# Optimization experiments

Hardware: AMD Instinct MI355X
Metric: run time of the kernel (lower is better)

## Reference

```python
import jax, jax.numpy as jnp
import numpy as np

EMB_DIM = 256
NUM_EMB = 2048
COM_COEF = 0.25


def setup_inputs() -> dict:
    key = jax.random.key(0)
    k1, k2 = jax.random.split(key)
    x = jax.random.normal(k1, (64, 32, 32, EMB_DIM), dtype=jnp.float32)
    # VarianceScaling(uniform) over (emb_dim, num_emb): limit = sqrt(3*scale/fan_in)
    limit = float(np.sqrt(3.0 / EMB_DIM))
    codebook = jax.random.uniform(k2, (EMB_DIM, NUM_EMB), dtype=jnp.float32,
                                  minval=-limit, maxval=limit)
    return {"x": x, "codebook": codebook}


def reference(x, codebook):
    original_shape = x.shape
    flat = jnp.reshape(x, (-1, EMB_DIM))  # [N, D]
    sim = jnp.matmul(flat, codebook)
    dists = (jnp.sum(jnp.square(flat), axis=-1, keepdims=True)
             + jnp.sum(jnp.square(codebook), axis=0)
             - 2.0 * sim)
    indexes = jnp.argmin(dists, axis=-1)  # [N]
    encodings = jax.nn.one_hot(indexes, NUM_EMB, dtype=flat.dtype)  # [N, num_emb]
    quantized = jnp.matmul(encodings, codebook.T)  # [N, D]
    quantized = jnp.reshape(quantized, original_shape)

    latent_loss = jnp.square(jax.lax.stop_gradient(x) - quantized)
    commitment_loss = jnp.square(jax.lax.stop_gradient(quantized) - x)
    loss = jnp.mean(latent_loss + COM_COEF * commitment_loss)

    # straight-through estimator
    quantized_st = x + jax.lax.stop_gradient(quantized - x)

    avg_probs = jnp.mean(encodings, axis=0)
    perplexity = jnp.exp(-jnp.sum(avg_probs * jnp.log(avg_probs + 1e-10)))
    return quantized_st, loss, perplexity
```

## Files before the change

kernel.cpp:

```cpp
#include <hip/hip_runtime.h>
#include <hip/hip_fp16.h>
#include <math.h>

#define EMB_DIM 256
#define NUM_EMB 2048
#define N_ROWS  65536
#define N_ELEM  16777216
#define EPS_GAP 8e-3f

#define IDX_OFF    0
#define XSQ_OFF    65536
#define ESQ_OFF    131072
#define ESQH_OFF   133120
#define HIST_OFF   135168
#define BKT_OFF    137216
#define CNT_OFF    137472
#define FLG_OFF    137473
#define CBT_OFF    262144
#define CBTH_OFF   786432

typedef __attribute__((ext_vector_type(8))) _Float16 half8;
typedef __attribute__((ext_vector_type(4))) float f32x4;
typedef unsigned int u32;

__device__ __forceinline__ void gl_lds16(const void* g, void* l) {
    __builtin_amdgcn_global_load_lds(
        (const __attribute__((address_space(1))) u32*)g,
        (__attribute__((address_space(3))) u32*)l, 16, 0, 0);
}

__global__ __launch_bounds__(256) void prep_all(
    const float* __restrict__ x, const float* __restrict__ cb,
    float* __restrict__ esq, float* __restrict__ esqh,
    float* __restrict__ cbT, __half* __restrict__ cbTh,
    __half* __restrict__ xh, float* __restrict__ xsq) {
    __shared__ float lt[64][65];
    const int bid = blockIdx.x;
    const int t = threadIdx.x;
    if (bid < 8) {
        int e = bid * 256 + t;
        float s0 = 0.f, s1 = 0.f, s2 = 0.f, s3 = 0.f;
        float h0 = 0.f, h1 = 0.f, h2 = 0.f, h3 = 0.f;
        for (int d = 0; d < EMB_DIM; d += 4) {
            float c0 = cb[(d + 0) * NUM_EMB + e];
            float c1 = cb[(d + 1) * NUM_EMB + e];
            float c2 = cb[(d + 2) * NUM_EMB + e];
            float c3 = cb[(d + 3) * NUM_EMB + e];
            s0 = fmaf(c0, c0, s0); s1 = fmaf(c1, c1, s1);
            s2 = fmaf(c2, c2, s2); s3 = fmaf(c3, c3, s3);
            float q0 = __half2float(__float2half(c0));
            float q1 = __half2float(__float2half(c1));
            float q2 = __half2float(__float2half(c2));
            float q3 = __half2float(__float2half(c3));
            h0 = fmaf(q0, q0, h0); h1 = fmaf(q1, q1, h1);
            h2 = fmaf(q2, q2, h2); h3 = fmaf(q3, q3, h3);
        }
        esq[e]  = (s0 + s1) + (s2 + s3);
        esqh[e] = (h0 + h1) + (h2 + h3);
    } else if (bid < 136) {
        int b = bid - 8;
        int et = (b & 31) * 64;
        int dt = (b >> 5) * 64;
        #pragma unroll
        for (int p = 0; p < 4; ++p) {
            int d  = p * 16 + (t >> 4);
            int e4 = (t & 15) * 4;
            const float4 v = *(const float4*)&cb[(dt + d) * NUM_EMB + et + e4];
            lt[d][e4] = v.x; lt[d][e4 + 1] = v.y; lt[d][e4 + 2] = v.z; lt[d][e4 + 3] = v.w;
        }
        __syncthreads();
        #pragma unroll
        for (int p = 0; p < 4; ++p) {
            int e  = p * 16 + (t >> 4);
            int d4 = (t & 15) * 4;
            float a[4] = {lt[d4][e], lt[d4 + 1][e], lt[d4 + 2][e], lt[d4 + 3][e]};
            *(float4*)&cbT[(et + e) * EMB_DIM + dt + d4] = make_float4(a[0], a[1], a[2], a[3]);
            unsigned short hb[4];
            #pragma unroll
            for (int i = 0; i < 4; ++i)
                hb[i] = __half_as_ushort(__float2half(a[i]));
            *(ushort4*)&cbTh[(et + e) * EMB_DIM + dt + d4] = make_ushort4(hb[0], hb[1], hb[2], hb[3]);
        }
    } else {
        int b = bid - 136;
        int row = b * 4 + (t >> 6);
        int c = (t & 63) * 4;
        const float4 v = *(const float4*)&x[row * EMB_DIM + c];
        float a[4] = {v.x, v.y, v.z, v.w};
        unsigned short hb[4];
        float s = 0.f;
        #pragma unroll
        for (int i = 0; i < 4; ++i) {
            hb[i] = __half_as_ushort(__float2half(a[i]));
            s = fmaf(a[i], a[i], s);
        }
        *(ushort4*)&xh[row * EMB_DIM + c] = make_ushort4(hb[0], hb[1], hb[2], hb[3]);
        #pragma unroll
        for (int o = 32; o > 0; o >>= 1) s += __shfl_down(s, o, 64);
        if ((t & 63) == 0) xsq[row] = s;
    }
}

#define BUFH 20480
__global__ __launch_bounds__(256, 2) void argmin_mfma(
    const __half* __restrict__ xh_, const __half* __restrict__ cbh_,
    const float* __restrict__ esqh,
    int* __restrict__ idx_out, int* __restrict__ cnt, int* __restrict__ flg) {

    __shared__ _Float16 ldsbuf[2 * BUFH];
    _Float16* lds = ldsbuf;

    const _Float16* xh  = (const _Float16*)xh_;
    const _Float16* cbh = (const _Float16*)cbh_;

    const int t = threadIdx.x;
    const int w = t >> 6, L = t & 63;
    const int wn = w * 64;
    const int lm = L & 15, lq = L >> 4;
    const int ph = (lm >> 1) & 3;
    const int rowbase = blockIdx.x * 64;

    const int srow = L >> 2;
    const int sq   = (L & 3) ^ ((L >> 3) & 3);

    const _Float16* pa  = xh + (size_t)(rowbase + w * 16 + srow) * EMB_DIM + sq * 8;
    const _Float16* pb0 = cbh + (size_t)(w * 16 + srow) * EMB_DIM + sq * 8;
    const int oA = (w * 16) * 32;
    const int oB = (w * 16) * 32;

    float best[16], b2[16];
    int   bi[16];
    #pragma unroll
    for (int s = 0; s < 16; ++s) { best[s] = 3.4e38f; b2[s] = 3.4e38f; bi[s] = 0; }

    #define STAGE(S_, bb) do {                                                   \
        const int nnt_ = (S_) >> 2;                                              \
        const int km_  = ((S_) & 3) * 64;                                        \
        const _Float16* pb_ = pb0 + (size_t)nnt_ * 256 * EMB_DIM + km_;          \
        gl_lds16(pa + km_,                 (bb) + oA);                           \
        gl_lds16(pa + km_ + 32,            (bb) + 2048 + oA);                    \
        gl_lds16(pb_ +   0 * EMB_DIM,      (bb) + 4096 + oB);                    \
        gl_lds16(pb_ +  64 * EMB_DIM,      (bb) + 4096 + oB + 2048);             \
        gl_lds16(pb_ + 128 * EMB_DIM,      (bb) + 4096 + oB + 4096);             \
        gl_lds16(pb_ + 192 * EMB_DIM,      (bb) + 4096 + oB + 6144);             \
        gl_lds16(pb_ +   0 * EMB_DIM + 32, (bb) + 12288 + oB);                   \
        gl_lds16(pb_ +  64 * EMB_DIM + 32, (bb) + 12288 + oB + 2048);            \
        gl_lds16(pb_ + 128 * EMB_DIM + 32, (bb) + 12288 + oB + 4096);            \
        gl_lds16(pb_ + 192 * EMB_DIM + 32, (bb) + 12288 + oB + 6144);            \
    } while (0)

    STAGE(0, lds);

    for (int nt = 0; nt < 8; ++nt) {
        float eq[4];
        #pragma unroll
        for (int g = 0; g < 4; ++g)
            eq[g] = esqh[nt * 256 + wn + g * 16 + lm];

        f32x4 acc[4][4];
        #pragma unroll
        for (int f = 0; f < 4; ++f)
            #pragma unroll
            for (int g = 0; g < 4; ++g)
                acc[f][g] = (f32x4){0.f, 0.f, 0.f, 0.f};

        for (int mt = 0; mt < 4; ++mt) {
            const int S = nt * 4 + mt;

            __builtin_amdgcn_sched_barrier(0);
            asm volatile("s_waitcnt vmcnt(0)" ::: "memory");
            __builtin_amdgcn_s_barrier();
            __builtin_amdgcn_sched_barrier(0);

            if (S < 31)
                STAGE(S + 1, lds + ((S + 1) & 1) * BUFH);

            const _Float16* bb = lds + (S & 1) * BUFH;

            half8 ah[2][4], bh[2][4];
            #pragma unroll
            for (int h = 0; h < 2; ++h)
                #pragma unroll
                for (int f = 0; f < 4; ++f)
                    ah[h][f] = *(const half8*)&bb[h * 2048 + (f * 16 + lm) * 32 + ((lq ^ ph) * 8)];
            #pragma unroll
            for (int h = 0; h < 2; ++h)
                #pragma unroll
                for (int g = 0; g < 4; ++g)
                    bh[h][g] = *(const half8*)&bb[4096 + h * 8192 + (wn + g * 16 + lm) * 32 + ((lq ^ ph) * 8)];

            asm volatile("s_waitcnt lgkmcnt(0)" ::: "memory");
            __builtin_amdgcn_sched_barrier(0);
            __builtin_amdgcn_s_barrier();
            __builtin_amdgcn_sched_barrier(0);

            __builtin_amdgcn_s_setprio(1);
            #pragma unroll
            for (int h = 0; h < 2; ++h)
                #pragma unroll
                for (int f = 0; f < 4; ++f)
                    #pragma unroll
                    for (int g = 0; g < 4; ++g)
                        acc[f][g] = __builtin_amdgcn_mfma_f32_16x16x32_f16(ah[h][f], bh[h][g], acc[f][g], 0, 0, 0);
            __builtin_amdgcn_s_setprio(0);
        }

        #pragma unroll
        for (int g = 0; g < 4; ++g) {
            int col = nt * 256 + wn + g * 16 + lm;
            #pragma unroll
            for (int f = 0; f < 4; ++f)
                #pragma unroll
                for (int r = 0; r < 4; ++r) {
                    int s = f * 4 + r;
                    float v = fmaf(-2.0f, acc[f][g][r], eq[g]);
                    float bo = best[s];
                    b2[s]   = fminf(b2[s], fmaxf(bo, v));
                    best[s] = fminf(bo, v);
                    bi[s]   = (v < bo) ? col : bi[s];
                }
        }
    }
    #undef STAGE

    __syncthreads();
    float* smemf = (float*)ldsbuf;
    float* rd = smemf;
    int*   ri = (int*)(smemf + 4160);
    float* r2 = smemf + 8320;
    #pragma unroll
    for (int f = 0; f < 4; ++f)
        #pragma unroll
        for (int r = 0; r < 4; ++r) {
            int row = f * 16 + lq * 4 + r;
            int c = w * 16 + lm;
            rd[row * 65 + c] = best[f * 4 + r];
            ri[row * 65 + c] = bi[f * 4 + r];
            r2[row * 65 + c] = b2[f * 4 + r];
        }
    __syncthreads();
    if (t < 64) {
        int row = t;
        float g1 = rd[row * 65]; int gi = ri[row * 65]; float g2 = r2[row * 65];
        for (int c = 1; c < 64; ++c) {
            float d = rd[row * 65 + c]; int ic = ri[row * 65 + c]; float d2 = r2[row * 65 + c];
            if (d < g1 || (d == g1 && ic < gi)) { g2 = fminf(g1, d2); g1 = d; gi = ic; }
            else g2 = fminf(g2, d);
        }
        idx_out[rowbase + row] = gi;
        if (g2 - g1 < EPS_GAP) {
            int p = atomicAdd(cnt, 1);
            flg[p] = rowbase + row;
        }
    }
}

__global__ __launch_bounds__(256) void fallback_k(const float* __restrict__ x,
                                                  const float* __restrict__ cb,
                                                  const float* __restrict__ xsq,
                                                  const float* __restrict__ esq,
                                                  const int* __restrict__ cnt,
                                                  const int* __restrict__ rows,
                                                  int* __restrict__ idx) {
    __shared__ float xr[4][256];
    __shared__ float sd[4][256];
    __shared__ int   si[4][256];
    int t = threadIdx.x;
    int n = *cnt;
    for (int base = blockIdx.x * 4; base < n; base += gridDim.x * 4) {
        int rws[4];
        #pragma unroll
        for (int r = 0; r < 4; ++r) {
            int fi = base + r;
            rws[r] = rows[(fi < n) ? fi : (n - 1)];
        }
        __syncthreads();
        #pragma unroll
        for (int r = 0; r < 4; ++r) xr[r][t] = x[(size_t)rws[r] * EMB_DIM + t];
        __syncthreads();

        float bd[4]; int bidx[4];
        #pragma unroll
        for (int r = 0; r < 4; ++r) { bd[r] = 3.4e38f; bidx[r] = 0x7fffffff; }

        for (int j = 0; j < 8; ++j) {
            int e = j * 256 + t;
            float s0[4], s1[4], s2[4], s3[4];
            #pragma unroll
            for (int r = 0; r < 4; ++r) { s0[r] = 0.f; s1[r] = 0.f; s2[r] = 0.f; s3[r] = 0.f; }
            for (int d = 0; d < EMB_DIM; d += 4) {
                float c0 = cb[(size_t)(d + 0) * NUM_EMB + e];
                float c1 = cb[(size_t)(d + 1) * NUM_EMB + e];
                float c2 = cb[(size_t)(d + 2) * NUM_EMB + e];
                float c3 = cb[(size_t)(d + 3) * NUM_EMB + e];
                #pragma unroll
                for (int r = 0; r < 4; ++r) {
                    const float4 xv = *(const float4*)&xr[r][d];
                    s0[r] = fmaf(xv.x, c0, s0[r]);
                    s1[r] = fmaf(xv.y, c1, s1[r]);
                    s2[r] = fmaf(xv.z, c2, s2[r]);
                    s3[r] = fmaf(xv.w, c3, s3[r]);
                }
            }
            float eqv = esq[e];
            #pragma unroll
            for (int r = 0; r < 4; ++r) {
                float sim = (s0[r] + s1[r]) + (s2[r] + s3[r]);
                float dd = (xsq[rws[r]] + eqv) - 2.0f * sim;
                if (dd < bd[r]) { bd[r] = dd; bidx[r] = e; }
            }
        }
        #pragma unroll
        for (int r = 0; r < 4; ++r) { sd[r][t] = bd[r]; si[r][t] = bidx[r]; }
        __syncthreads();
        for (int r = 0; r < 4; ++r) {
            for (int stp = 128; stp > 0; stp >>= 1) {
                if (t < stp) {
                    if (sd[r][t + stp] < sd[r][t] ||
                        (sd[r][t + stp] == sd[r][t] && si[r][t + stp] < si[r][t])) {
                        sd[r][t] = sd[r][t + stp]; si[r][t] = si[r][t + stp];
                    }
                }
                __syncthreads();
            }
        }
        if (t == 0) {
            #pragma unroll
            for (int r = 0; r < 4; ++r) idx[rws[r]] = si[r][0];
        }
    }
}

__global__ __launch_bounds__(256) void quant_k(const float* __restrict__ x,
                                               const float* __restrict__ cbT,
                                               const int* __restrict__ idx,
                                               float* __restrict__ out,
                                               float* __restrict__ bkt,
                                               int* __restrict__ hist) {
    int t = threadIdx.x;
    int row = blockIdx.x * 4 + (t >> 6);
    int c = (t & 63) * 4;
    int e = idx[row];
    const float4 q  = *(const float4*)&cbT[(size_t)e * EMB_DIM + c];
    const float4 xv = *(const float4*)&x[(size_t)row * EMB_DIM + c];
    float4 o;
    o.x = xv.x + (q.x - xv.x); o.y = xv.y + (q.y - xv.y);
    o.z = xv.z + (q.z - xv.z); o.w = xv.w + (q.w - xv.w);
    *(float4*)&out[(size_t)row * EMB_DIM + c] = o;
    float dx = xv.x - q.x, dy = xv.y - q.y, dz = xv.z - q.z, dw = xv.w - q.w;
    float val = fmaf(dx, dx, 0.f);
    val = fmaf(dy, dy, val);
    val = fmaf(dz, dz, val);
    val = fmaf(dw, dw, val);
    #pragma unroll
    for (int o2 = 32; o2 > 0; o2 >>= 1) val += __shfl_down(val, o2, 64);
    if ((t & 63) == 0) {
        atomicAdd(&bkt[row & 255], val);
        atomicAdd(&hist[e], 1);
    }
}

__global__ __launch_bounds__(256) void final_k(const float* __restrict__ bkt,
                                               const int* __restrict__ hist,
                                               float* __restrict__ out) {
    int t = threadIdx.x;
    double ls = (double)bkt[t];
    double ps = 0.0;
    for (int i = t; i < NUM_EMB; i += 256) {
        double p = (double)hist[i] / (double)N_ROWS;
        ps += p * log(p + 1e-10);
    }
    __shared__ double sdd[256], spp[256];
    sdd[t] = ls; spp[t] = ps;
    __syncthreads();
    for (int s = 128; s > 0; s >>= 1) {
        if (t < s) { sdd[t] += sdd[t + s]; spp[t] += spp[t + s]; }
        __syncthreads();
    }
    if (t == 0) {
        out[N_ELEM + 0] = (float)(1.25 * sdd[0] / (double)N_ELEM);
        out[N_ELEM + 1] = (float)exp(-spp[0]);
    }
}

extern "C" void kernel_launch(void* const* d_in, const int* in_sizes, int n_in,
                              void* d_out, int out_size, void* d_ws, size_t ws_size,
                              hipStream_t stream) {
    const float* x  = (const float*)d_in[0];
    const float* cb = (const float*)d_in[1];
    float* out = (float*)d_out;

    float* ws_f = (float*)d_ws;
    int*   ws_i = (int*)d_ws;
    int*   idx  = ws_i + IDX_OFF;
    float* xsq  = ws_f + XSQ_OFF;
    float* esq  = ws_f + ESQ_OFF;
    float* esqh = ws_f + ESQH_OFF;
    int*   hist = ws_i + HIST_OFF;
    float* bkt  = ws_f + BKT_OFF;
    int*   cnt  = ws_i + CNT_OFF;
    int*   flg  = ws_i + FLG_OFF;
    float* cbT  = ws_f + CBT_OFF;
    __half* cbTh = (__half*)(ws_f + CBTH_OFF);

    __half* xh = (__half*)d_out;

    hipMemsetAsync((char*)d_ws + (size_t)HIST_OFF * 4, 0,
                   (NUM_EMB + 256 + 1) * sizeof(float), stream);

    prep_all<<<8 + 128 + N_ROWS / 4, 256, 0, stream>>>(x, cb, esq, esqh, cbT, cbTh, xh, xsq);
    argmin_mfma<<<N_ROWS / 64, 256, 0, stream>>>(xh, cbTh, esqh, idx, cnt, flg);
    fallback_k<<<512, 256, 0, stream>>>(x, cb, xsq, esq, cnt, flg, idx);
    quant_k<<<N_ROWS / 4, 256, 0, stream>>>(x, cbT, idx, out, bkt, hist);
    final_k<<<1, 256, 0, stream>>>(bkt, hist, out);
}
```

Baseline: 431.6 us.

## Fuse fallback argmin with quantization and halve prep grid for x conversion

Merges the exact-distance fallback kernel and the quantize/loss kernel into one persistent 512-block kernel. Flagged rows are quantized immediately after their exact argmin, reusing the row already held in shared memory. A per-row byte mask lets the grid-stride pass skip rows that were already handled. The x-to-half prep now has each block process 8 rows instead of 4, halving the block count. This removes one kernel launch and the dependency gap between the two kernels, at the cost of an extra memset and a 512-block grid-stride loop instead of a wide one-row-per-wave launch.

```diff
diff --git a/kernel.cpp b/kernel.cpp
--- a/kernel.cpp
+++ b/kernel.cpp
@@ -16,6 +16,7 @@
 #define BKT_OFF    137216
 #define CNT_OFF    137472
 #define FLG_OFF    137473
+#define FLGB_OFF   204800
 #define CBT_OFF    262144
 #define CBTH_OFF   786432
 
@@ -83,21 +84,24 @@
         }
     } else {
         int b = bid - 136;
-        int row = b * 4 + (t >> 6);
-        int c = (t & 63) * 4;
-        const float4 v = *(const float4*)&x[row * EMB_DIM + c];
-        float a[4] = {v.x, v.y, v.z, v.w};
-        unsigned short hb[4];
-        float s = 0.f;
-        #pragma unroll
-        for (int i = 0; i < 4; ++i) {
-            hb[i] = __half_as_ushort(__float2half(a[i]));
-            s = fmaf(a[i], a[i], s);
-        }
-        *(ushort4*)&xh[row * EMB_DIM + c] = make_ushort4(hb[0], hb[1], hb[2], hb[3]);
-        #pragma unroll
-        for (int o = 32; o > 0; o >>= 1) s += __shfl_down(s, o, 64);
-        if ((t & 63) == 0) xsq[row] = s;
+        #pragma unroll
+        for (int gdup = 0; gdup < 2; ++gdup) {
+            int row = b * 8 + gdup * 4 + (t >> 6);
+            int c = (t & 63) * 4;
+            const float4 v = *(const float4*)&x[(size_t)row * EMB_DIM + c];
+            float a[4] = {v.x, v.y, v.z, v.w};
+            unsigned short hb[4];
+            float s = 0.f;
+            #pragma unroll
+            for (int i = 0; i < 4; ++i) {
+                hb[i] = __half_as_ushort(__float2half(a[i]));
+                s = fmaf(a[i], a[i], s);
+            }
+            *(ushort4*)&xh[(size_t)row * EMB_DIM + c] = make_ushort4(hb[0], hb[1], hb[2], hb[3]);
+            #pragma unroll
+            for (int o = 32; o > 0; o >>= 1) s += __shfl_down(s, o, 64);
+            if ((t & 63) == 0) xsq[row] = s;
+        }
     }
 }
 
@@ -105,7 +109,8 @@
 __global__ __launch_bounds__(256, 2) void argmin_mfma(
     const __half* __restrict__ xh_, const __half* __restrict__ cbh_,
     const float* __restrict__ esqh,
-    int* __restrict__ idx_out, int* __restrict__ cnt, int* __restrict__ flg) {
+    int* __restrict__ idx_out, int* __restrict__ cnt, int* __restrict__ flg,
+    unsigned char* __restrict__ flagged) {
 
     __shared__ _Float16 ldsbuf[2 * BUFH];
     _Float16* lds = ldsbuf;
@@ -251,22 +256,26 @@
         if (g2 - g1 < EPS_GAP) {
             int p = atomicAdd(cnt, 1);
             flg[p] = rowbase + row;
-        }
-    }
-}
-
-__global__ __launch_bounds__(256) void fallback_k(const float* __restrict__ x,
-                                                  const float* __restrict__ cb,
-                                                  const float* __restrict__ xsq,
-                                                  const float* __restrict__ esq,
-                                                  const int* __restrict__ cnt,
-                                                  const int* __restrict__ rows,
-                                                  int* __restrict__ idx) {
+            flagged[rowbase + row] = 1;
+        }
+    }
+}
+
+__global__ __launch_bounds__(256) void fallback_quant_k(
+    const float* __restrict__ x, const float* __restrict__ cb,
+    const float* __restrict__ cbT,
+    const float* __restrict__ xsq, const float* __restrict__ esq,
+    const int* __restrict__ cnt, const int* __restrict__ rows,
+    const unsigned char* __restrict__ flagged,
+    int* __restrict__ idx, float* __restrict__ out,
+    float* __restrict__ bkt, int* __restrict__ hist) {
     __shared__ float xr[4][256];
     __shared__ float sd[4][256];
     __shared__ int   si[4][256];
-    int t = threadIdx.x;
+    const int t = threadIdx.x;
+    const int w = t >> 6, L = t & 63;
     int n = *cnt;
+
     for (int base = blockIdx.x * 4; base < n; base += gridDim.x * 4) {
         int rws[4];
         #pragma unroll
@@ -324,39 +333,53 @@
                 __syncthreads();
             }
         }
-        if (t == 0) {
-            #pragma unroll
-            for (int r = 0; r < 4; ++r) idx[rws[r]] = si[r][0];
-        }
-    }
-}
-
-__global__ __launch_bounds__(256) void quant_k(const float* __restrict__ x,
-                                               const float* __restrict__ cbT,
-                                               const int* __restrict__ idx,
-                                               float* __restrict__ out,
-                                               float* __restrict__ bkt,
-                                               int* __restrict__ hist) {
-    int t = threadIdx.x;
-    int row = blockIdx.x * 4 + (t >> 6);
-    int c = (t & 63) * 4;
-    int e = idx[row];
-    const float4 q  = *(const float4*)&cbT[(size_t)e * EMB_DIM + c];
-    const float4 xv = *(const float4*)&x[(size_t)row * EMB_DIM + c];
-    float4 o;
-    o.x = xv.x + (q.x - xv.x); o.y = xv.y + (q.y - xv.y);
-    o.z = xv.z + (q.z - xv.z); o.w = xv.w + (q.w - xv.w);
-    *(float4*)&out[(size_t)row * EMB_DIM + c] = o;
-    float dx = xv.x - q.x, dy = xv.y - q.y, dz = xv.z - q.z, dw = xv.w - q.w;
-    float val = fmaf(dx, dx, 0.f);
-    val = fmaf(dy, dy, val);
-    val = fmaf(dz, dz, val);
-    val = fmaf(dw, dw, val);
-    #pragma unroll
-    for (int o2 = 32; o2 > 0; o2 >>= 1) val += __shfl_down(val, o2, 64);
-    if ((t & 63) == 0) {
-        atomicAdd(&bkt[row & 255], val);
-        atomicAdd(&hist[e], 1);
+        if (base + w < n) {
+            int rowg = rws[w];
+            int e = si[w][0];
+            if (L == 0) idx[rowg] = e;
+            int c = L * 4;
+            const float4 q  = *(const float4*)&cbT[(size_t)e * EMB_DIM + c];
+            const float4 xv = *(const float4*)&xr[w][c];
+            float4 o;
+            o.x = xv.x + (q.x - xv.x); o.y = xv.y + (q.y - xv.y);
+            o.z = xv.z + (q.z - xv.z); o.w = xv.w + (q.w - xv.w);
+            *(float4*)&out[(size_t)rowg * EMB_DIM + c] = o;
+            float dx = xv.x - q.x, dy = xv.y - q.y, dz = xv.z - q.z, dw = xv.w - q.w;
+            float val = fmaf(dx, dx, 0.f);
+            val = fmaf(dy, dy, val);
+            val = fmaf(dz, dz, val);
+            val = fmaf(dw, dw, val);
+            #pragma unroll
+            for (int o2 = 32; o2 > 0; o2 >>= 1) val += __shfl_down(val, o2, 64);
+            if (L == 0) {
+                atomicAdd(&bkt[rowg & 255], val);
+                atomicAdd(&hist[e], 1);
+            }
+        }
+    }
+
+    for (int qb = blockIdx.x; qb < N_ROWS / 4; qb += gridDim.x) {
+        int row = qb * 4 + w;
+        if (flagged[row]) continue;
+        int e = idx[row];
+        int c = L * 4;
+        const float4 q  = *(const float4*)&cbT[(size_t)e * EMB_DIM + c];
+        const float4 xv = *(const float4*)&x[(size_t)row * EMB_DIM + c];
+        float4 o;
+        o.x = xv.x + (q.x - xv.x); o.y = xv.y + (q.y - xv.y);
+        o.z = xv.z + (q.z - xv.z); o.w = xv.w + (q.w - xv.w);
+        *(float4*)&out[(size_t)row * EMB_DIM + c] = o;
+        float dx = xv.x - q.x, dy = xv.y - q.y, dz = xv.z - q.z, dw = xv.w - q.w;
+        float val = fmaf(dx, dx, 0.f);
+        val = fmaf(dy, dy, val);
+        val = fmaf(dz, dz, val);
+        val = fmaf(dw, dw, val);
+        #pragma unroll
+        for (int o2 = 32; o2 > 0; o2 >>= 1) val += __shfl_down(val, o2, 64);
+        if (L == 0) {
+            atomicAdd(&bkt[row & 255], val);
+            atomicAdd(&hist[e], 1);
+        }
     }
 }
 
@@ -400,6 +423,7 @@
     float* bkt  = ws_f + BKT_OFF;
     int*   cnt  = ws_i + CNT_OFF;
     int*   flg  = ws_i + FLG_OFF;
+    unsigned char* flagged = (unsigned char*)(ws_i + FLGB_OFF);
     float* cbT  = ws_f + CBT_OFF;
     __half* cbTh = (__half*)(ws_f + CBTH_OFF);
 
@@ -407,10 +431,11 @@
 
     hipMemsetAsync((char*)d_ws + (size_t)HIST_OFF * 4, 0,
                    (NUM_EMB + 256 + 1) * sizeof(float), stream);
-
-    prep_all<<<8 + 128 + N_ROWS / 4, 256, 0, stream>>>(x, cb, esq, esqh, cbT, cbTh, xh, xsq);
-    argmin_mfma<<<N_ROWS / 64, 256, 0, stream>>>(xh, cbTh, esqh, idx, cnt, flg);
-    fallback_k<<<512, 256, 0, stream>>>(x, cb, xsq, esq, cnt, flg, idx);
-    quant_k<<<N_ROWS / 4, 256, 0, stream>>>(x, cbT, idx, out, bkt, hist);
+    hipMemsetAsync((char*)d_ws + (size_t)FLGB_OFF * 4, 0, N_ROWS, stream);
+
+    prep_all<<<8 + 128 + N_ROWS / 8, 256, 0, stream>>>(x, cb, esq, esqh, cbT, cbTh, xh, xsq);
+    argmin_mfma<<<N_ROWS / 64, 256, 0, stream>>>(xh, cbTh, esqh, idx, cnt, flg, flagged);
+    fallback_quant_k<<<512, 256, 0, stream>>>(x, cb, cbT, xsq, esq, cnt, flg, flagged,
+                                              idx, out, bkt, hist);
     final_k<<<1, 256, 0, stream>>>(bkt, hist, out);
 }
```

After: 395.4 us. -8.4%, faster.
